# Performance work log

Hardware: AMD Instinct MI355X
Metric: run time of the kernel (lower is better)

Reference implementation:

```python
import jax, jax.numpy as jnp
import numpy as np

MUL0, MUL1 = 128, 64
DIM1 = MUL0 + 3 * MUL1          # 320 = dim of 128x0e + 64x1o
DIM2 = 4                        # 1x0e + 1x1o
WDIM, H = 16, 64
# per-instruction weight sizes (mul_in2 = 1), e3nn instruction order
N1 = MUL0 * MUL0                # (0e x 0e -> 0e)
N2 = MUL0 * MUL1                # (0e x 1o -> 1o)
N3 = MUL1 * MUL1                # (1o x 0e -> 1o)
N4 = MUL1 * MUL0                # (1o x 1o -> 0e)
WNUMEL = N1 + N2 + N3 + N4      # 36864
FAN = MUL0 + MUL1               # summed fan-in per output slice = 192
PW0 = float(np.sqrt(1.0 / FAN))         # path weight, component/element norm, l_out=0
PW1 = float(np.sqrt(3.0 / FAN))         # l_out=1 (alpha = 2l+1 = 3)
INV_SQRT3 = float(1.0 / np.sqrt(3.0))   # wigner_3j(1,1,0)/(0,1,1)/(1,0,1) entries
SQRT_K = float(1.0 / np.sqrt(FAN))      # tp_rescale correction (output divided by this)


def setup_inputs() -> dict:
    key = jax.random.key(0)
    ks = jax.random.split(key, 8)
    N = 4096

    def lin(k, fin, fout):
        k1, k2 = jax.random.split(k)
        lim = 1.0 / np.sqrt(fin)
        W = jax.random.uniform(k1, (fin, fout), minval=-lim, maxval=lim, dtype=jnp.float32)
        b = jax.random.uniform(k2, (fout,), minval=-lim, maxval=lim, dtype=jnp.float32)
        return W, b

    W0, b0 = lin(ks[3], WDIM, H)
    W1, b1 = lin(ks[4], H, H)
    W2, b2 = lin(ks[5], H, WNUMEL)
    return {
        "data_in1": jax.random.normal(ks[0], (N, DIM1), dtype=jnp.float32),
        "data_in2": jax.random.normal(ks[1], (N, DIM2), dtype=jnp.float32),
        "weight": jax.random.normal(ks[2], (N, WDIM), dtype=jnp.float32),
        "W0": W0, "b0": b0, "W1": W1, "b1": b1, "W2": W2, "b2": b2,
        "bias": jax.random.uniform(ks[6], (MUL0,), minval=-SQRT_K, maxval=SQRT_K, dtype=jnp.float32),
    }


def _forward(data_in1, data_in2, weight, W0, b0, W1, b1, W2, b2, bias):
    # weight-generating MLP: 16 -> 64 -> 64 -> weight_numel
    h = jax.nn.relu(weight @ W0 + b0)
    h = jax.nn.relu(h @ W1 + b1)
    w = h @ W2 + b2                                   # [N, WNUMEL] per-sample tp weights
    # split inputs into irrep blocks
    s1 = data_in1[:, :MUL0]                           # [N,128]  128x0e
    v1 = data_in1[:, MUL0:].reshape(-1, MUL1, 3)      # [N,64,3]  64x1o
    s2 = data_in2[:, 0]                               # [N]       1x0e
    v2 = data_in2[:, 1:4]                             # [N,3]     1x1o
    # per-instruction weight views (uvw with v=1 collapsed)
    Wa = w[:, :N1].reshape(-1, MUL0, MUL0)                   # 0e x 0e -> 0e
    Wb = w[:, N1:N1 + N2].reshape(-1, MUL0, MUL1)            # 0e x 1o -> 1o
    Wc = w[:, N1 + N2:N1 + N2 + N3].reshape(-1, MUL1, MUL1)  # 1o x 0e -> 1o
    Wd = w[:, N1 + N2 + N3:].reshape(-1, MUL1, MUL0)         # 1o x 1o -> 0e
    dot12 = jnp.einsum('eui,ei->eu', v1, v2)          # [N,64]
    # scalar (0e) output slice: paths Wa (w3j=1) and Wd (w3j = delta/sqrt(3))
    out0 = PW0 * (jnp.einsum('euw,eu->ew', Wa, s1) * s2[:, None]
                  + INV_SQRT3 * jnp.einsum('euw,eu->ew', Wd, dot12))
    # vector (1o) output slice: paths Wb and Wc (w3j = delta/sqrt(3))
    out1 = PW1 * INV_SQRT3 * (
        jnp.einsum('euw,eu->ew', Wb, s1)[:, :, None] * v2[:, None, :]
        + jnp.einsum('euw,eui->ewi', Wc, v1) * s2[:, None, None])
    out = jnp.concatenate([out0, out1.reshape(-1, 3 * MUL1)], axis=1)  # [N,320]
    out = out / SQRT_K                                # tp_rescale: divide by sqrt_k correction
    out = out.at[:, :MUL0].add(bias)                  # bias added on 0e slice only
    return out


def reference(data_in1, data_in2, weight, W0, b0, W1, b1, W2, b2, bias):
    return _forward(data_in1, data_in2, weight, W0, b0, W1, b1, W2, b2, bias)
```

## Files before the change

### kernel.cpp

```cpp
#include <hip/hip_runtime.h>
#include <hip/hip_bf16.h>

typedef __attribute__((ext_vector_type(8))) short short8;
typedef __attribute__((ext_vector_type(4))) float f32x4;

constexpr int N1 = 16384, N2 = 8192, N3 = 4096;
constexpr int WN = 36864;
constexpr float ISQ3 = 0.57735026918962576451f;

__device__ __forceinline__ unsigned short f2bf(float f) {
  unsigned u = __builtin_bit_cast(unsigned, f);
  u += 0x7fffu + ((u >> 16) & 1u);
  return (unsigned short)(u >> 16);
}

#define MFMA(a, b, c) __builtin_amdgcn_mfma_f32_16x16x32_bf16((a), (b), (c), 0, 0, 0)

__global__ __launch_bounds__(256)
void k_prep(const float* __restrict__ wgt, const float* __restrict__ W0,
            const float* __restrict__ b0, const float* __restrict__ W1,
            const float* __restrict__ b1, const float* __restrict__ W2,
            const float* __restrict__ b2, const float* __restrict__ bias,
            const float* __restrict__ d1, const float* __restrict__ d2,
            float* __restrict__ H, unsigned short* __restrict__ Bp,
            float* __restrict__ sAg, float* __restrict__ sBg,
            float* __restrict__ sDg, float* __restrict__ sCg,
            float* __restrict__ d2T, float* __restrict__ out) {
  __shared__ __align__(16) float shm[10400];
  const int bid = blockIdx.x;
  const int tid = threadIdx.x;

  if (bid < 512) {
    float* s1s = shm;
    float* v1s = shm + 1024;
    float* dts = shm + 2560;
    float* s2s = shm + 3072;
    float* v2s = shm + 3080;
    const int e0 = bid * 8;
    for (int x = tid; x < 8 * 320; x += 256) {
      int e = x / 320, c = x % 320;
      float v = d1[(size_t)(e0 + e) * 320 + c];
      if (c < 128) s1s[e * 128 + c] = v;
      else { int q = c - 128; v1s[(e * 64 + q / 3) * 3 + q % 3] = v; }
    }
    if (tid < 32) {
      int e = tid >> 2, c = tid & 3;
      float v = d2[(size_t)(e0 + e) * 4 + c];
      if (c == 0) s2s[e] = v; else v2s[e * 3 + c - 1] = v;
    }
    __syncthreads();
    for (int x = tid; x < 8 * 64; x += 256) {
      int e = x >> 6, u = x & 63;
      dts[e * 64 + u] = v1s[(e * 64 + u) * 3] * v2s[e * 3] +
                        v1s[(e * 64 + u) * 3 + 1] * v2s[e * 3 + 1] +
                        v1s[(e * 64 + u) * 3 + 2] * v2s[e * 3 + 2];
    }
    __syncthreads();
    for (int c = tid; c < 320; c += 256) {
      if (c < 128) {
        const int w = c;
        float ta[8] = {0,0,0,0,0,0,0,0}, td[8] = {0,0,0,0,0,0,0,0};
        for (int u = 0; u < 128; ++u) {
          float bv = b2[u * 128 + w];
#pragma unroll
          for (int e = 0; e < 8; ++e) ta[e] = fmaf(s1s[e * 128 + u], bv, ta[e]);
        }
        for (int u = 0; u < 64; ++u) {
          float bv = b2[N1 + N2 + N3 + u * 128 + w];
#pragma unroll
          for (int e = 0; e < 8; ++e) td[e] = fmaf(dts[e * 64 + u], bv, td[e]);
        }
        const float bw = bias[w];
#pragma unroll
        for (int e = 0; e < 8; ++e)
          out[(size_t)(e0 + e) * 320 + c] = fmaf(s2s[e], ta[e], ISQ3 * td[e]) + bw;
      } else {
        const int q = c - 128, w = q / 3, i = q % 3;
        float tb[8] = {0,0,0,0,0,0,0,0}, tc[8] = {0,0,0,0,0,0,0,0};
        for (int u = 0; u < 128; ++u) {
          float bv = b2[N1 + u * 64 + w];
#pragma unroll
          for (int e = 0; e < 8; ++e) tb[e] = fmaf(s1s[e * 128 + u], bv, tb[e]);
        }
        for (int u = 0; u < 64; ++u) {
          float bv = b2[N1 + N2 + u * 64 + w];
#pragma unroll
          for (int e = 0; e < 8; ++e) tc[e] = fmaf(v1s[(e * 64 + u) * 3 + i], bv, tc[e]);
        }
#pragma unroll
        for (int e = 0; e < 8; ++e)
          out[(size_t)(e0 + e) * 320 + c] = tb[e] * v2s[e * 3 + i] + tc[e] * s2s[e];
      }
    }
  } else if (bid < 1664) {
    const int g = (bid - 512) * 256 + tid;
    const int lane = g & 63;
    const int nth = g >> 6;
    const int kh = nth & 1, nt = nth >> 1;
    const int n = nt * 16 + (lane & 15);
    const int k0 = kh * 32 + (lane >> 4) * 8;
    short8 v;
#pragma unroll
    for (int q = 0; q < 8; ++q) v[q] = (short)f2bf(W2[(size_t)(k0 + q) * WN + n]);
    *(short8*)(Bp + (size_t)g * 8) = v;
  } else if (bid < 2688) {
    float* h0s = shm;
    const int r = tid >> 6, jj = tid & 63;
    const int e = (bid - 1664) * 4 + r;
    float a = b0[jj];
#pragma unroll
    for (int i = 0; i < 16; ++i) a = fmaf(wgt[e * 16 + i], W0[i * 64 + jj], a);
    h0s[r * 64 + jj] = fmaxf(a, 0.f);
    __syncthreads();
    float a1 = b1[jj];
#pragma unroll
    for (int i = 0; i < 64; ++i) a1 = fmaf(h0s[r * 64 + i], W1[i * 64 + jj], a1);
    H[e * 64 + jj] = fmaxf(a1, 0.f);
  } else {
    float* d1s = shm;
    float* d2s = shm + 10272;
    const int e0 = (bid - 2688) * 32;
    for (int x = tid; x < 32 * 320; x += 256) {
      int e = x / 320, c = x % 320;
      d1s[e * 321 + c] = d1[(size_t)(e0 + e) * 320 + c];
    }
    if (tid < 128) d2s[tid] = d2[(size_t)e0 * 4 + tid];
    __syncthreads();
    const int e = tid & 31;
    const float s2 = d2s[e * 4 + 0];
    const float w1 = d2s[e * 4 + 1], w2 = d2s[e * 4 + 2], w3 = d2s[e * 4 + 3];
    for (int row = (tid >> 5); row < 516; row += 8) {
      float v; float* dst;
      if (row < 128)      { v = d1s[e * 321 + row] * s2;            dst = sAg + (size_t)row * 4096; }
      else if (row < 256) { v = d1s[e * 321 + (row - 128)];         dst = sBg + (size_t)(row - 128) * 4096; }
      else if (row < 320) { int u = row - 256;
        v = ISQ3 * (d1s[e * 321 + 128 + 3 * u] * w1 + d1s[e * 321 + 129 + 3 * u] * w2 +
                    d1s[e * 321 + 130 + 3 * u] * w3);               dst = sDg + (size_t)u * 4096; }
      else if (row < 512) { v = d1s[e * 321 + 128 + (row - 320)] * s2; dst = sCg + (size_t)(row - 320) * 4096; }
      else                { v = d2s[e * 4 + (row - 512)];           dst = d2T + (size_t)(row - 512) * 4096; }
      dst[e0 + e] = v;
    }
  }
}

__global__ __launch_bounds__(256, 3)
void k_main(const float* __restrict__ sAg, const float* __restrict__ sBg,
            const float* __restrict__ sDg, const float* __restrict__ sCg,
            const float* __restrict__ d2T, const float* __restrict__ H,
            const unsigned short* __restrict__ Bp, float* __restrict__ out) {
  __shared__ __align__(16) float lds[8704];
  const int bid = blockIdx.x, tid = threadIdx.x;
  const int wid = tid >> 6, lane = tid & 63;
  const int nl = lane & 15, grp = lane >> 4;
  const short8* Bp8 = (const short8*)Bp;
  const f32x4 Z = {0.f, 0.f, 0.f, 0.f};

  if (bid < 512) {
    const int j = bid & 7, tile = bid >> 3, e0 = tile * 64;
    short8 h00, h01, h10, h11, h20, h21, h30, h31;
    {
      const float* hp; short8 v0, v1;
#define LOADH(EF, N0, N1_)                                                     \
      hp = H + (size_t)(e0 + 16 * EF + nl) * 64 + grp * 8;                     \
      _Pragma("unroll") for (int q = 0; q < 8; ++q) {                          \
        v0[q] = (short)f2bf(hp[q]); v1[q] = (short)f2bf(hp[32 + q]); }         \
      N0 = v0; N1_ = v1;
      LOADH(0, h00, h01) LOADH(1, h10, h11) LOADH(2, h20, h21) LOADH(3, h30, h31)
#undef LOADH
    }
    const int uA0 = wid * 32, uD0 = wid * 16;
    const short8* pA = Bp8 + (size_t)(uA0 * 8 + j) * 128 + lane;
    const short8* pD = Bp8 + (size_t)(1792 + uD0 * 8 + j) * 128 + lane;
    const float* qA0 = sAg + (size_t)uA0 * 4096 + e0 + nl;
    const float* qA1 = qA0 + 4096;
    const float* qD  = sDg + (size_t)uD0 * 4096 + e0 + nl;

    short8 A00 = pA[0], A01 = pA[64], A10 = pA[1024], A11 = pA[1088]; pA += 2048;
    short8 D00 = pD[0], D01 = pD[64]; pD += 1024;
    float sa0 = qA0[0], sa1 = qA0[16], sa2 = qA0[32], sa3 = qA0[48];
    float sa4 = qA1[0], sa5 = qA1[16], sa6 = qA1[32], sa7 = qA1[48]; qA0 += 8192; qA1 += 8192;
    float sd0 = qD[0], sd1 = qD[16], sd2 = qD[32], sd3 = qD[48]; qD += 4096;
    short8 B00 = pA[0], B01 = pA[64], B10 = pA[1024], B11 = pA[1088]; pA += 2048;
    short8 E00 = pD[0], E01 = pD[64]; pD += 1024;
    float ta0 = qA0[0], ta1 = qA0[16], ta2 = qA0[32], ta3 = qA0[48];
    float ta4 = qA1[0], ta5 = qA1[16], ta6 = qA1[32], ta7 = qA1[48]; qA0 += 8192; qA1 += 8192;
    float td0 = qD[0], td1 = qD[16], td2 = qD[32], td3 = qD[48]; qD += 4096;

    f32x4 accA[4] = {Z, Z, Z, Z};
    f32x4 accD[4] = {Z, Z, Z, Z};

#define QUAD(P0, P1, S0, S1, S2, S3, AC) do { f32x4 t_;                        \
    t_ = Z; t_ = MFMA(P0, h00, t_); t_ = MFMA(P1, h01, t_); AC[0] += (S0) * t_; \
    t_ = Z; t_ = MFMA(P0, h10, t_); t_ = MFMA(P1, h11, t_); AC[1] += (S1) * t_; \
    t_ = Z; t_ = MFMA(P0, h20, t_); t_ = MFMA(P1, h21, t_); AC[2] += (S2) * t_; \
    t_ = Z; t_ = MFMA(P0, h30, t_); t_ = MFMA(P1, h31, t_); AC[3] += (S3) * t_; } while (0)

#pragma unroll
    for (int t = 0; t < 16; t += 2) {
      QUAD(A00, A01, sa0, sa1, sa2, sa3, accA);
      QUAD(A10, A11, sa4, sa5, sa6, sa7, accA);
      QUAD(D00, D01, sd0, sd1, sd2, sd3, accD);
      if (t < 14) {
        A00 = pA[0]; A01 = pA[64]; A10 = pA[1024]; A11 = pA[1088]; pA += 2048;
        D00 = pD[0]; D01 = pD[64]; pD += 1024;
        sa0 = qA0[0]; sa1 = qA0[16]; sa2 = qA0[32]; sa3 = qA0[48];
        sa4 = qA1[0]; sa5 = qA1[16]; sa6 = qA1[32]; sa7 = qA1[48]; qA0 += 8192; qA1 += 8192;
        sd0 = qD[0]; sd1 = qD[16]; sd2 = qD[32]; sd3 = qD[48]; qD += 4096;
      }
      QUAD(B00, B01, ta0, ta1, ta2, ta3, accA);
      QUAD(B10, B11, ta4, ta5, ta6, ta7, accA);
      QUAD(E00, E01, td0, td1, td2, td3, accD);
      if (t < 13) {
        B00 = pA[0]; B01 = pA[64]; B10 = pA[1024]; B11 = pA[1088]; pA += 2048;
        E00 = pD[0]; E01 = pD[64]; pD += 1024;
        ta0 = qA0[0]; ta1 = qA0[16]; ta2 = qA0[32]; ta3 = qA0[48];
        ta4 = qA1[0]; ta5 = qA1[16]; ta6 = qA1[32]; ta7 = qA1[48]; qA0 += 8192; qA1 += 8192;
        td0 = qD[0]; td1 = qD[16]; td2 = qD[32]; td3 = qD[48]; qD += 4096;
      }
    }
#undef QUAD

#pragma unroll
    for (int eF = 0; eF < 4; ++eF) {
      f32x4 fin = accA[eF] + accD[eF];
      *(f32x4*)&lds[wid * 1280 + (16 * eF + nl) * 20 + grp * 4] = fin;
    }
    __syncthreads();
    {
      const int e = tid >> 2, w4 = (tid & 3) * 4;
      f32x4 s = Z;
#pragma unroll
      for (int wv = 0; wv < 4; ++wv) s += *(const f32x4*)&lds[wv * 1280 + e * 20 + w4];
      f32x4* op = (f32x4*)(out + (size_t)(e0 + e) * 320 + j * 16 + w4);
      *op = *op + s;
    }
  } else {
    const int idx = bid - 512;
    const int j = idx & 3;
    const int tile = ((idx >> 3) << 1) + ((idx >> 2) & 1);
    const int e0 = tile * 32;
    short8 h00, h01, h10, h11;
    {
      const float* hp; short8 v0, v1;
#define LOADH(EF, N0, N1_)                                                     \
      hp = H + (size_t)(e0 + 16 * EF + nl) * 64 + grp * 8;                     \
      _Pragma("unroll") for (int q = 0; q < 8; ++q) {                          \
        v0[q] = (short)f2bf(hp[q]); v1[q] = (short)f2bf(hp[32 + q]); }         \
      N0 = v0; N1_ = v1;
      LOADH(0, h00, h01) LOADH(1, h10, h11)
#undef LOADH
    }
    const int uB0 = wid * 32, uC0 = wid * 16;
    const short8* pB = Bp8 + (size_t)(1024 + uB0 * 4 + j) * 128 + lane;
    const short8* pC = Bp8 + (size_t)(1536 + uC0 * 4 + j) * 128 + lane;
    const float* qB0 = sBg + (size_t)uB0 * 4096 + e0 + nl;
    const float* qB1 = qB0 + 4096;
    const float* qC0 = sCg + (size_t)(uC0 * 3) * 4096 + e0 + nl;
    const float* qC1 = qC0 + 4096;
    const float* qC2 = qC0 + 8192;

    short8 A00 = pB[0], A01 = pB[64], A10 = pB[512], A11 = pB[576]; pB += 1024;
    short8 C00 = pC[0], C01 = pC[64]; pC += 512;
    float sb0 = qB0[0], sb1 = qB0[16], sb2 = qB1[0], sb3 = qB1[16]; qB0 += 8192; qB1 += 8192;
    float sc00 = qC0[0], sc01 = qC0[16], sc10 = qC1[0], sc11 = qC1[16],
          sc20 = qC2[0], sc21 = qC2[16]; qC0 += 12288; qC1 += 12288; qC2 += 12288;
    short8 B00 = pB[0], B01 = pB[64], B10 = pB[512], B11 = pB[576]; pB += 1024;
    short8 E00 = pC[0], E01 = pC[64]; pC += 512;
    float tb0 = qB0[0], tb1 = qB0[16], tb2 = qB1[0], tb3 = qB1[16]; qB0 += 8192; qB1 += 8192;
    float tc00 = qC0[0], tc01 = qC0[16], tc10 = qC1[0], tc11 = qC1[16],
          tc20 = qC2[0], tc21 = qC2[16]; qC0 += 12288; qC1 += 12288; qC2 += 12288;

    f32x4 accB[2] = {Z, Z};
    f32x4 accC0[2] = {Z, Z}, accC1[2] = {Z, Z}, accC2[2] = {Z, Z};

#define DUO(P0, P1, S0, S1) do { f32x4 t_;                                     \
    t_ = Z; t_ = MFMA(P0, h00, t_); t_ = MFMA(P1, h01, t_); accB[0] += (S0) * t_; \
    t_ = Z; t_ = MFMA(P0, h10, t_); t_ = MFMA(P1, h11, t_); accB[1] += (S1) * t_; } while (0)
#define CTRIO(P0, P1, X00, X01, X10, X11, X20, X21) do { f32x4 u0_, u1_;       \
    u0_ = Z; u0_ = MFMA(P0, h00, u0_); u0_ = MFMA(P1, h01, u0_);               \
    u1_ = Z; u1_ = MFMA(P0, h10, u1_); u1_ = MFMA(P1, h11, u1_);               \
    accC0[0] += (X00) * u0_; accC0[1] += (X01) * u1_;                          \
    accC1[0] += (X10) * u0_; accC1[1] += (X11) * u1_;                          \
    accC2[0] += (X20) * u0_; accC2[1] += (X21) * u1_; } while (0)

#pragma unroll
    for (int t = 0; t < 16; t += 2) {
      DUO(A00, A01, sb0, sb1);
      DUO(A10, A11, sb2, sb3);
      CTRIO(C00, C01, sc00, sc01, sc10, sc11, sc20, sc21);
      if (t < 14) {
        A00 = pB[0]; A01 = pB[64]; A10 = pB[512]; A11 = pB[576]; pB += 1024;
        C00 = pC[0]; C01 = pC[64]; pC += 512;
        sb0 = qB0[0]; sb1 = qB0[16]; sb2 = qB1[0]; sb3 = qB1[16]; qB0 += 8192; qB1 += 8192;
        sc00 = qC0[0]; sc01 = qC0[16]; sc10 = qC1[0]; sc11 = qC1[16];
        sc20 = qC2[0]; sc21 = qC2[16]; qC0 += 12288; qC1 += 12288; qC2 += 12288;
      }
      DUO(B00, B01, tb0, tb1);
      DUO(B10, B11, tb2, tb3);
      CTRIO(E00, E01, tc00, tc01, tc10, tc11, tc20, tc21);
      if (t < 13) {
        B00 = pB[0]; B01 = pB[64]; B10 = pB[512]; B11 = pB[576]; pB += 1024;
        E00 = pC[0]; E01 = pC[64]; pC += 512;
        tb0 = qB0[0]; tb1 = qB0[16]; tb2 = qB1[0]; tb3 = qB1[16]; qB0 += 8192; qB1 += 8192;
        tc00 = qC0[0]; tc01 = qC0[16]; tc10 = qC1[0]; tc11 = qC1[16];
        tc20 = qC2[0]; tc21 = qC2[16]; qC0 += 12288; qC1 += 12288; qC2 += 12288;
      }
    }
#undef DUO
#undef CTRIO

#pragma unroll
    for (int eF = 0; eF < 2; ++eF)
#pragma unroll
      for (int r = 0; r < 4; ++r) {
        f32x4 v = {accB[eF][r], accC0[eF][r], accC1[eF][r], accC2[eF][r]};
        *(f32x4*)&lds[wid * 2176 + (16 * eF + nl) * 68 + (grp * 4 + r) * 4] = v;
      }
    __syncthreads();
    for (int p = tid; p < 512; p += 256) {
      const int e = p >> 4, w = p & 15;
      f32x4 s = Z;
#pragma unroll
      for (int wv = 0; wv < 4; ++wv) s += *(const f32x4*)&lds[wv * 2176 + e * 68 + w * 4];
      const float v20 = d2T[4096 + e0 + e], v21 = d2T[8192 + e0 + e], v22 = d2T[12288 + e0 + e];
      float* op = out + (size_t)(e0 + e) * 320 + 128 + (size_t)(j * 16 + w) * 3;
      op[0] += s[0] * v20 + s[1];
      op[1] += s[0] * v21 + s[2];
      op[2] += s[0] * v22 + s[3];
    }
  }
}

extern "C" void kernel_launch(void* const* d_in, const int* in_sizes, int n_in,
                              void* d_out, int out_size, void* d_ws, size_t ws_size,
                              hipStream_t stream) {
  const float* d1   = (const float*)d_in[0];
  const float* d2   = (const float*)d_in[1];
  const float* wgt  = (const float*)d_in[2];
  const float* W0   = (const float*)d_in[3];
  const float* b0   = (const float*)d_in[4];
  const float* W1   = (const float*)d_in[5];
  const float* b1   = (const float*)d_in[6];
  const float* W2   = (const float*)d_in[7];
  const float* b2   = (const float*)d_in[8];
  const float* bias = (const float*)d_in[9];
  float* out = (float*)d_out;

  char* ws = (char*)d_ws;
  float* H           = (float*)(ws);
  unsigned short* Bp = (unsigned short*)(ws + (1u << 20));
  float* sAg         = (float*)(ws + (6u << 20));
  float* sBg         = (float*)(ws + (8u << 20));
  float* sDg         = (float*)(ws + (10u << 20));
  float* sCg         = (float*)(ws + (11u << 20));
  float* d2T         = (float*)(ws + (14u << 20));

  k_prep<<<2816, 256, 0, stream>>>(wgt, W0, b0, W1, b1, W2, b2, bias, d1, d2,
                                   H, Bp, sAg, sBg, sDg, sCg, d2T, out);
  k_main<<<1024, 256, 0, stream>>>(sAg, sBg, sDg, sCg, d2T, H, Bp, out);
}
```

Baseline: 73.86 us.

## Fold per-sample scalars into MFMA operand and merge all paths into one block

Moves the per-edge scalar multiply into the bf16 H operand: each edge's scaled H row is packed with v_cvt_pk_bf16_f32, so the Wa, Wb and Wd paths accumulate directly in MFMA accumulators instead of scaling each partial product. The Wc path still scales afterwards. One 512-thread block now handles all four paths for a 32-edge tile and half of the output columns, and the two waves sharing each slice are reduced through LDS. It also adds s_setprio around the MFMA bursts and cuts the grid to 256 blocks, which trades per-step VALU packing and lower occupancy for fewer scalar multiply-adds and fewer launched blocks.

```diff
diff --git a/kernel.cpp b/kernel.cpp
--- a/kernel.cpp
+++ b/kernel.cpp
@@ -3,6 +3,7 @@
 
 typedef __attribute__((ext_vector_type(8))) short short8;
 typedef __attribute__((ext_vector_type(4))) float f32x4;
+typedef __attribute__((ext_vector_type(4))) unsigned uint4v;
 
 constexpr int N1 = 16384, N2 = 8192, N3 = 4096;
 constexpr int WN = 36864;
@@ -14,7 +15,22 @@
   return (unsigned short)(u >> 16);
 }
 
+__device__ __forceinline__ unsigned pkbf(float a, float b) {
+  unsigned r;
+  asm("v_cvt_pk_bf16_f32 %0, %1, %2" : "=v"(r) : "v"(a), "v"(b));
+  return r;
+}
+
 #define MFMA(a, b, c) __builtin_amdgcn_mfma_f32_16x16x32_bf16((a), (b), (c), 0, 0, 0)
+
+#define SYNTH(S, HF, G0, G1) do {                                                   \
+    uint4v w0_, w1_;                                                                \
+    w0_[0] = pkbf((S)*HF[0],  (S)*HF[1]);   w0_[1] = pkbf((S)*HF[2],  (S)*HF[3]);   \
+    w0_[2] = pkbf((S)*HF[4],  (S)*HF[5]);   w0_[3] = pkbf((S)*HF[6],  (S)*HF[7]);   \
+    w1_[0] = pkbf((S)*HF[8],  (S)*HF[9]);   w1_[1] = pkbf((S)*HF[10], (S)*HF[11]);  \
+    w1_[2] = pkbf((S)*HF[12], (S)*HF[13]);  w1_[3] = pkbf((S)*HF[14], (S)*HF[15]);  \
+    G0 = __builtin_bit_cast(short8, w0_);   G1 = __builtin_bit_cast(short8, w1_);   \
+  } while (0)
 
 __global__ __launch_bounds__(256)
 void k_prep(const float* __restrict__ wgt, const float* __restrict__ W0,
@@ -143,190 +159,255 @@
   }
 }
 
-__global__ __launch_bounds__(256, 3)
+
+#define ADBODY(F0,F1,F2,F3,F4,F5,F6,F7,S0,S1) do {                             \
+    short8 g00,g01,g10,g11;                                                    \
+    SYNTH(S0, hf0, g00, g01); SYNTH(S1, hf1, g10, g11);                        \
+    __builtin_amdgcn_s_setprio(1);                                             \
+    a00 = MFMA(F0,g00,a00); a00 = MFMA(F1,g01,a00);                            \
+    a01 = MFMA(F0,g10,a01); a01 = MFMA(F1,g11,a01);                            \
+    a10 = MFMA(F2,g00,a10); a10 = MFMA(F3,g01,a10);                            \
+    a11 = MFMA(F2,g10,a11); a11 = MFMA(F3,g11,a11);                            \
+    a20 = MFMA(F4,g00,a20); a20 = MFMA(F5,g01,a20);                            \
+    a21 = MFMA(F4,g10,a21); a21 = MFMA(F5,g11,a21);                            \
+    a30 = MFMA(F6,g00,a30); a30 = MFMA(F7,g01,a30);                            \
+    a31 = MFMA(F6,g10,a31); a31 = MFMA(F7,g11,a31);                            \
+    __builtin_amdgcn_s_setprio(0);                                             \
+  } while (0)
+
+#define BBODY(F0,F1,F2,F3,S0,S1) do {                                          \
+    short8 g00,g01,g10,g11;                                                    \
+    SYNTH(S0, hf0, g00, g01); SYNTH(S1, hf1, g10, g11);                        \
+    __builtin_amdgcn_s_setprio(1);                                             \
+    b00 = MFMA(F0,g00,b00); b00 = MFMA(F1,g01,b00);                            \
+    b01 = MFMA(F0,g10,b01); b01 = MFMA(F1,g11,b01);                            \
+    b10 = MFMA(F2,g00,b10); b10 = MFMA(F3,g01,b10);                            \
+    b11 = MFMA(F2,g10,b11); b11 = MFMA(F3,g11,b11);                            \
+    __builtin_amdgcn_s_setprio(0);                                             \
+  } while (0)
+
+#define CBODY(F0,F1,F2,F3,S00,S01,S10,S11,S20,S21) do {                        \
+    __builtin_amdgcn_s_setprio(1);                                             \
+    f32x4 t00 = Zv; t00 = MFMA(F0,hb00,t00); t00 = MFMA(F1,hb01,t00);          \
+    f32x4 t01 = Zv; t01 = MFMA(F0,hb10,t01); t01 = MFMA(F1,hb11,t01);          \
+    f32x4 t10 = Zv; t10 = MFMA(F2,hb00,t10); t10 = MFMA(F3,hb01,t10);          \
+    f32x4 t11 = Zv; t11 = MFMA(F2,hb10,t11); t11 = MFMA(F3,hb11,t11);          \
+    __builtin_amdgcn_s_setprio(0);                                             \
+    c000 += S00*t00; c001 += S01*t01; c010 += S00*t10; c011 += S01*t11;        \
+    c100 += S10*t00; c101 += S11*t01; c110 += S10*t10; c111 += S11*t11;        \
+    c200 += S20*t00; c201 += S21*t01; c210 += S20*t10; c211 += S21*t11;        \
+  } while (0)
+
+__global__ __launch_bounds__(512, 2)
 void k_main(const float* __restrict__ sAg, const float* __restrict__ sBg,
             const float* __restrict__ sDg, const float* __restrict__ sCg,
             const float* __restrict__ d2T, const float* __restrict__ H,
             const unsigned short* __restrict__ Bp, float* __restrict__ out) {
-  __shared__ __align__(16) float lds[8704];
-  const int bid = blockIdx.x, tid = threadIdx.x;
+  __shared__ __align__(16) float buf[4 * 32 * 136];
+  const int tid = threadIdx.x;
   const int wid = tid >> 6, lane = tid & 63;
   const int nl = lane & 15, grp = lane >> 4;
+  const int h = (blockIdx.x >> 2) & 1;
+  const int tile = (blockIdx.x >> 3) * 4 + (blockIdx.x & 3);
+  const int e0 = tile * 32;
   const short8* Bp8 = (const short8*)Bp;
-  const f32x4 Z = {0.f, 0.f, 0.f, 0.f};
-
-  if (bid < 512) {
-    const int j = bid & 7, tile = bid >> 3, e0 = tile * 64;
-    short8 h00, h01, h10, h11, h20, h21, h30, h31;
-    {
-      const float* hp; short8 v0, v1;
-#define LOADH(EF, N0, N1_)                                                     \
-      hp = H + (size_t)(e0 + 16 * EF + nl) * 64 + grp * 8;                     \
-      _Pragma("unroll") for (int q = 0; q < 8; ++q) {                          \
-        v0[q] = (short)f2bf(hp[q]); v1[q] = (short)f2bf(hp[32 + q]); }         \
-      N0 = v0; N1_ = v1;
-      LOADH(0, h00, h01) LOADH(1, h10, h11) LOADH(2, h20, h21) LOADH(3, h30, h31)
-#undef LOADH
-    }
-    const int uA0 = wid * 32, uD0 = wid * 16;
-    const short8* pA = Bp8 + (size_t)(uA0 * 8 + j) * 128 + lane;
-    const short8* pD = Bp8 + (size_t)(1792 + uD0 * 8 + j) * 128 + lane;
-    const float* qA0 = sAg + (size_t)uA0 * 4096 + e0 + nl;
-    const float* qA1 = qA0 + 4096;
-    const float* qD  = sDg + (size_t)uD0 * 4096 + e0 + nl;
-
-    short8 A00 = pA[0], A01 = pA[64], A10 = pA[1024], A11 = pA[1088]; pA += 2048;
-    short8 D00 = pD[0], D01 = pD[64]; pD += 1024;
-    float sa0 = qA0[0], sa1 = qA0[16], sa2 = qA0[32], sa3 = qA0[48];
-    float sa4 = qA1[0], sa5 = qA1[16], sa6 = qA1[32], sa7 = qA1[48]; qA0 += 8192; qA1 += 8192;
-    float sd0 = qD[0], sd1 = qD[16], sd2 = qD[32], sd3 = qD[48]; qD += 4096;
-    short8 B00 = pA[0], B01 = pA[64], B10 = pA[1024], B11 = pA[1088]; pA += 2048;
-    short8 E00 = pD[0], E01 = pD[64]; pD += 1024;
-    float ta0 = qA0[0], ta1 = qA0[16], ta2 = qA0[32], ta3 = qA0[48];
-    float ta4 = qA1[0], ta5 = qA1[16], ta6 = qA1[32], ta7 = qA1[48]; qA0 += 8192; qA1 += 8192;
-    float td0 = qD[0], td1 = qD[16], td2 = qD[32], td3 = qD[48]; qD += 4096;
-
-    f32x4 accA[4] = {Z, Z, Z, Z};
-    f32x4 accD[4] = {Z, Z, Z, Z};
-
-#define QUAD(P0, P1, S0, S1, S2, S3, AC) do { f32x4 t_;                        \
-    t_ = Z; t_ = MFMA(P0, h00, t_); t_ = MFMA(P1, h01, t_); AC[0] += (S0) * t_; \
-    t_ = Z; t_ = MFMA(P0, h10, t_); t_ = MFMA(P1, h11, t_); AC[1] += (S1) * t_; \
-    t_ = Z; t_ = MFMA(P0, h20, t_); t_ = MFMA(P1, h21, t_); AC[2] += (S2) * t_; \
-    t_ = Z; t_ = MFMA(P0, h30, t_); t_ = MFMA(P1, h31, t_); AC[3] += (S3) * t_; } while (0)
-
-#pragma unroll
-    for (int t = 0; t < 16; t += 2) {
-      QUAD(A00, A01, sa0, sa1, sa2, sa3, accA);
-      QUAD(A10, A11, sa4, sa5, sa6, sa7, accA);
-      QUAD(D00, D01, sd0, sd1, sd2, sd3, accD);
-      if (t < 14) {
-        A00 = pA[0]; A01 = pA[64]; A10 = pA[1024]; A11 = pA[1088]; pA += 2048;
-        D00 = pD[0]; D01 = pD[64]; pD += 1024;
-        sa0 = qA0[0]; sa1 = qA0[16]; sa2 = qA0[32]; sa3 = qA0[48];
-        sa4 = qA1[0]; sa5 = qA1[16]; sa6 = qA1[32]; sa7 = qA1[48]; qA0 += 8192; qA1 += 8192;
-        sd0 = qD[0]; sd1 = qD[16]; sd2 = qD[32]; sd3 = qD[48]; qD += 4096;
-      }
-      QUAD(B00, B01, ta0, ta1, ta2, ta3, accA);
-      QUAD(B10, B11, ta4, ta5, ta6, ta7, accA);
-      QUAD(E00, E01, td0, td1, td2, td3, accD);
-      if (t < 13) {
-        B00 = pA[0]; B01 = pA[64]; B10 = pA[1024]; B11 = pA[1088]; pA += 2048;
-        E00 = pD[0]; E01 = pD[64]; pD += 1024;
-        ta0 = qA0[0]; ta1 = qA0[16]; ta2 = qA0[32]; ta3 = qA0[48];
-        ta4 = qA1[0]; ta5 = qA1[16]; ta6 = qA1[32]; ta7 = qA1[48]; qA0 += 8192; qA1 += 8192;
-        td0 = qD[0]; td1 = qD[16]; td2 = qD[32]; td3 = qD[48]; qD += 4096;
-      }
-    }
-#undef QUAD
-
-#pragma unroll
-    for (int eF = 0; eF < 4; ++eF) {
-      f32x4 fin = accA[eF] + accD[eF];
-      *(f32x4*)&lds[wid * 1280 + (16 * eF + nl) * 20 + grp * 4] = fin;
-    }
-    __syncthreads();
-    {
-      const int e = tid >> 2, w4 = (tid & 3) * 4;
-      f32x4 s = Z;
-#pragma unroll
-      for (int wv = 0; wv < 4; ++wv) s += *(const f32x4*)&lds[wv * 1280 + e * 20 + w4];
-      f32x4* op = (f32x4*)(out + (size_t)(e0 + e) * 320 + j * 16 + w4);
-      *op = *op + s;
-    }
-  } else {
-    const int idx = bid - 512;
-    const int j = idx & 3;
-    const int tile = ((idx >> 3) << 1) + ((idx >> 2) & 1);
-    const int e0 = tile * 32;
-    short8 h00, h01, h10, h11;
-    {
-      const float* hp; short8 v0, v1;
-#define LOADH(EF, N0, N1_)                                                     \
-      hp = H + (size_t)(e0 + 16 * EF + nl) * 64 + grp * 8;                     \
-      _Pragma("unroll") for (int q = 0; q < 8; ++q) {                          \
-        v0[q] = (short)f2bf(hp[q]); v1[q] = (short)f2bf(hp[32 + q]); }         \
-      N0 = v0; N1_ = v1;
-      LOADH(0, h00, h01) LOADH(1, h10, h11)
-#undef LOADH
-    }
-    const int uB0 = wid * 32, uC0 = wid * 16;
-    const short8* pB = Bp8 + (size_t)(1024 + uB0 * 4 + j) * 128 + lane;
-    const short8* pC = Bp8 + (size_t)(1536 + uC0 * 4 + j) * 128 + lane;
-    const float* qB0 = sBg + (size_t)uB0 * 4096 + e0 + nl;
-    const float* qB1 = qB0 + 4096;
-    const float* qC0 = sCg + (size_t)(uC0 * 3) * 4096 + e0 + nl;
-    const float* qC1 = qC0 + 4096;
-    const float* qC2 = qC0 + 8192;
-
-    short8 A00 = pB[0], A01 = pB[64], A10 = pB[512], A11 = pB[576]; pB += 1024;
-    short8 C00 = pC[0], C01 = pC[64]; pC += 512;
-    float sb0 = qB0[0], sb1 = qB0[16], sb2 = qB1[0], sb3 = qB1[16]; qB0 += 8192; qB1 += 8192;
-    float sc00 = qC0[0], sc01 = qC0[16], sc10 = qC1[0], sc11 = qC1[16],
-          sc20 = qC2[0], sc21 = qC2[16]; qC0 += 12288; qC1 += 12288; qC2 += 12288;
-    short8 B00 = pB[0], B01 = pB[64], B10 = pB[512], B11 = pB[576]; pB += 1024;
-    short8 E00 = pC[0], E01 = pC[64]; pC += 512;
-    float tb0 = qB0[0], tb1 = qB0[16], tb2 = qB1[0], tb3 = qB1[16]; qB0 += 8192; qB1 += 8192;
-    float tc00 = qC0[0], tc01 = qC0[16], tc10 = qC1[0], tc11 = qC1[16],
-          tc20 = qC2[0], tc21 = qC2[16]; qC0 += 12288; qC1 += 12288; qC2 += 12288;
-
-    f32x4 accB[2] = {Z, Z};
-    f32x4 accC0[2] = {Z, Z}, accC1[2] = {Z, Z}, accC2[2] = {Z, Z};
-
-#define DUO(P0, P1, S0, S1) do { f32x4 t_;                                     \
-    t_ = Z; t_ = MFMA(P0, h00, t_); t_ = MFMA(P1, h01, t_); accB[0] += (S0) * t_; \
-    t_ = Z; t_ = MFMA(P0, h10, t_); t_ = MFMA(P1, h11, t_); accB[1] += (S1) * t_; } while (0)
-#define CTRIO(P0, P1, X00, X01, X10, X11, X20, X21) do { f32x4 u0_, u1_;       \
-    u0_ = Z; u0_ = MFMA(P0, h00, u0_); u0_ = MFMA(P1, h01, u0_);               \
-    u1_ = Z; u1_ = MFMA(P0, h10, u1_); u1_ = MFMA(P1, h11, u1_);               \
-    accC0[0] += (X00) * u0_; accC0[1] += (X01) * u1_;                          \
-    accC1[0] += (X10) * u0_; accC1[1] += (X11) * u1_;                          \
-    accC2[0] += (X20) * u0_; accC2[1] += (X21) * u1_; } while (0)
-
-#pragma unroll
-    for (int t = 0; t < 16; t += 2) {
-      DUO(A00, A01, sb0, sb1);
-      DUO(A10, A11, sb2, sb3);
-      CTRIO(C00, C01, sc00, sc01, sc10, sc11, sc20, sc21);
-      if (t < 14) {
-        A00 = pB[0]; A01 = pB[64]; A10 = pB[512]; A11 = pB[576]; pB += 1024;
-        C00 = pC[0]; C01 = pC[64]; pC += 512;
-        sb0 = qB0[0]; sb1 = qB0[16]; sb2 = qB1[0]; sb3 = qB1[16]; qB0 += 8192; qB1 += 8192;
-        sc00 = qC0[0]; sc01 = qC0[16]; sc10 = qC1[0]; sc11 = qC1[16];
-        sc20 = qC2[0]; sc21 = qC2[16]; qC0 += 12288; qC1 += 12288; qC2 += 12288;
-      }
-      DUO(B00, B01, tb0, tb1);
-      DUO(B10, B11, tb2, tb3);
-      CTRIO(E00, E01, tc00, tc01, tc10, tc11, tc20, tc21);
-      if (t < 13) {
-        B00 = pB[0]; B01 = pB[64]; B10 = pB[512]; B11 = pB[576]; pB += 1024;
-        E00 = pC[0]; E01 = pC[64]; pC += 512;
-        tb0 = qB0[0]; tb1 = qB0[16]; tb2 = qB1[0]; tb3 = qB1[16]; qB0 += 8192; qB1 += 8192;
-        tc00 = qC0[0]; tc01 = qC0[16]; tc10 = qC1[0]; tc11 = qC1[16];
-        tc20 = qC2[0]; tc21 = qC2[16]; qC0 += 12288; qC1 += 12288; qC2 += 12288;
-      }
-    }
-#undef DUO
-#undef CTRIO
-
-#pragma unroll
-    for (int eF = 0; eF < 2; ++eF)
-#pragma unroll
-      for (int r = 0; r < 4; ++r) {
-        f32x4 v = {accB[eF][r], accC0[eF][r], accC1[eF][r], accC2[eF][r]};
-        *(f32x4*)&lds[wid * 2176 + (16 * eF + nl) * 68 + (grp * 4 + r) * 4] = v;
-      }
-    __syncthreads();
-    for (int p = tid; p < 512; p += 256) {
-      const int e = p >> 4, w = p & 15;
-      f32x4 s = Z;
-#pragma unroll
-      for (int wv = 0; wv < 4; ++wv) s += *(const f32x4*)&lds[wv * 2176 + e * 68 + w * 4];
+  const f32x4 Zv = {0.f, 0.f, 0.f, 0.f};
+
+  float hf0[16], hf1[16];
+  {
+    const float* hp0 = H + (size_t)(e0 + nl) * 64 + grp * 8;
+    const float* hp1 = H + (size_t)(e0 + 16 + nl) * 64 + grp * 8;
+    f32x4 x0 = *(const f32x4*)(hp0),      x1 = *(const f32x4*)(hp0 + 4);
+    f32x4 x2 = *(const f32x4*)(hp0 + 32), x3 = *(const f32x4*)(hp0 + 36);
+    f32x4 y0 = *(const f32x4*)(hp1),      y1 = *(const f32x4*)(hp1 + 4);
+    f32x4 y2 = *(const f32x4*)(hp1 + 32), y3 = *(const f32x4*)(hp1 + 36);
+#pragma unroll
+    for (int q = 0; q < 4; ++q) {
+      hf0[q] = x0[q]; hf0[4+q] = x1[q]; hf0[8+q] = x2[q]; hf0[12+q] = x3[q];
+      hf1[q] = y0[q]; hf1[4+q] = y1[q]; hf1[8+q] = y2[q]; hf1[12+q] = y3[q];
+    }
+  }
+
+  f32x4 a00=Zv,a01=Zv,a10=Zv,a11=Zv,a20=Zv,a21=Zv,a30=Zv,a31=Zv;
+
+  {
+    const int u0 = wid * 16;
+    const short8* pe = Bp8 + (size_t)(u0 * 8 + 4 * h) * 128 + lane;
+    const short8* po = pe + 1024;
+    const float* se = sAg + (size_t)u0 * 4096 + e0 + nl;
+    const float* so = se + 4096;
+    short8 Ea0=pe[0],Ea1=pe[64],Ea2=pe[128],Ea3=pe[192],Ea4=pe[256],Ea5=pe[320],Ea6=pe[384],Ea7=pe[448];
+    short8 Oa0=po[0],Oa1=po[64],Oa2=po[128],Oa3=po[192],Oa4=po[256],Oa5=po[320],Oa6=po[384],Oa7=po[448];
+    float sE0=se[0], sE1=se[16], sO0=so[0], sO1=so[16];
+#pragma unroll 2
+    for (int t = 0; t < 8; ++t) {
+      ADBODY(Ea0,Ea1,Ea2,Ea3,Ea4,Ea5,Ea6,Ea7, sE0,sE1);
+      pe += 2048; se += 8192;
+      Ea0=pe[0];Ea1=pe[64];Ea2=pe[128];Ea3=pe[192];Ea4=pe[256];Ea5=pe[320];Ea6=pe[384];Ea7=pe[448];
+      sE0=se[0]; sE1=se[16];
+      ADBODY(Oa0,Oa1,Oa2,Oa3,Oa4,Oa5,Oa6,Oa7, sO0,sO1);
+      po += 2048; so += 8192;
+      Oa0=po[0];Oa1=po[64];Oa2=po[128];Oa3=po[192];Oa4=po[256];Oa5=po[320];Oa6=po[384];Oa7=po[448];
+      sO0=so[0]; sO1=so[16];
+    }
+  }
+
+  f32x4 b00=Zv,b01=Zv,b10=Zv,b11=Zv;
+
+  {
+    const int u0 = wid * 16;
+    const short8* pe = Bp8 + (size_t)(1024 + u0 * 4 + 2 * h) * 128 + lane;
+    const short8* po = pe + 512;
+    const float* se = sBg + (size_t)u0 * 4096 + e0 + nl;
+    const float* so = se + 4096;
+    short8 Ea0=pe[0],Ea1=pe[64],Ea2=pe[128],Ea3=pe[192];
+    short8 Oa0=po[0],Oa1=po[64],Oa2=po[128],Oa3=po[192];
+    float sE0=se[0], sE1=se[16], sO0=so[0], sO1=so[16];
+#pragma unroll 2
+    for (int t = 0; t < 8; ++t) {
+      BBODY(Ea0,Ea1,Ea2,Ea3, sE0,sE1);
+      pe += 1024; se += 8192;
+      Ea0=pe[0];Ea1=pe[64];Ea2=pe[128];Ea3=pe[192];
+      sE0=se[0]; sE1=se[16];
+      BBODY(Oa0,Oa1,Oa2,Oa3, sO0,sO1);
+      po += 1024; so += 8192;
+      Oa0=po[0];Oa1=po[64];Oa2=po[128];Oa3=po[192];
+      sO0=so[0]; sO1=so[16];
+    }
+  }
+
+  {
+    const int u0 = wid * 8;
+    const short8* pe = Bp8 + (size_t)(1792 + u0 * 8 + 4 * h) * 128 + lane;
+    const short8* po = pe + 1024;
+    const float* se = sDg + (size_t)u0 * 4096 + e0 + nl;
+    const float* so = se + 4096;
+    short8 Ea0=pe[0],Ea1=pe[64],Ea2=pe[128],Ea3=pe[192],Ea4=pe[256],Ea5=pe[320],Ea6=pe[384],Ea7=pe[448];
+    short8 Oa0=po[0],Oa1=po[64],Oa2=po[128],Oa3=po[192],Oa4=po[256],Oa5=po[320],Oa6=po[384],Oa7=po[448];
+    float sE0=se[0], sE1=se[16], sO0=so[0], sO1=so[16];
+#pragma unroll 2
+    for (int t = 0; t < 4; ++t) {
+      ADBODY(Ea0,Ea1,Ea2,Ea3,Ea4,Ea5,Ea6,Ea7, sE0,sE1);
+      pe += 2048; se += 8192;
+      Ea0=pe[0];Ea1=pe[64];Ea2=pe[128];Ea3=pe[192];Ea4=pe[256];Ea5=pe[320];Ea6=pe[384];Ea7=pe[448];
+      sE0=se[0]; sE1=se[16];
+      ADBODY(Oa0,Oa1,Oa2,Oa3,Oa4,Oa5,Oa6,Oa7, sO0,sO1);
+      po += 2048; so += 8192;
+      Oa0=po[0];Oa1=po[64];Oa2=po[128];Oa3=po[192];Oa4=po[256];Oa5=po[320];Oa6=po[384];Oa7=po[448];
+      sO0=so[0]; sO1=so[16];
+    }
+  }
+
+  short8 hb00, hb01, hb10, hb11;
+  SYNTH(1.0f, hf0, hb00, hb01);
+  SYNTH(1.0f, hf1, hb10, hb11);
+  f32x4 c000=Zv,c001=Zv,c010=Zv,c011=Zv,c100=Zv,c101=Zv,c110=Zv,c111=Zv,c200=Zv,c201=Zv,c210=Zv,c211=Zv;
+  {
+    const int u0 = wid * 8;
+    const short8* pe = Bp8 + (size_t)(1536 + u0 * 4 + 2 * h) * 128 + lane;
+    const short8* po = pe + 512;
+    const float* sc0e = sCg + (size_t)(3 * u0) * 4096 + e0 + nl;
+    const float* sc1e = sc0e + 4096;
+    const float* sc2e = sc0e + 8192;
+    const float* sc0o = sc0e + 12288;
+    const float* sc1o = sc0e + 16384;
+    const float* sc2o = sc0e + 20480;
+    short8 Ea0=pe[0],Ea1=pe[64],Ea2=pe[128],Ea3=pe[192];
+    short8 Oa0=po[0],Oa1=po[64],Oa2=po[128],Oa3=po[192];
+    float sE00=sc0e[0],sE01=sc0e[16],sE10=sc1e[0],sE11=sc1e[16],sE20=sc2e[0],sE21=sc2e[16];
+    float sO00=sc0o[0],sO01=sc0o[16],sO10=sc1o[0],sO11=sc1o[16],sO20=sc2o[0],sO21=sc2o[16];
+#pragma unroll 2
+    for (int t = 0; t < 4; ++t) {
+      CBODY(Ea0,Ea1,Ea2,Ea3, sE00,sE01,sE10,sE11,sE20,sE21);
+      pe += 1024; sc0e += 24576; sc1e += 24576; sc2e += 24576;
+      Ea0=pe[0];Ea1=pe[64];Ea2=pe[128];Ea3=pe[192];
+      sE00=sc0e[0];sE01=sc0e[16];sE10=sc1e[0];sE11=sc1e[16];sE20=sc2e[0];sE21=sc2e[16];
+      CBODY(Oa0,Oa1,Oa2,Oa3, sO00,sO01,sO10,sO11,sO20,sO21);
+      po += 1024; sc0o += 24576; sc1o += 24576; sc2o += 24576;
+      Oa0=po[0];Oa1=po[64];Oa2=po[128];Oa3=po[192];
+      sO00=sc0o[0];sO01=sc0o[16];sO10=sc1o[0];sO11=sc1o[16];sO20=sc2o[0];sO21=sc2o[16];
+    }
+  }
+
+  {
+    f32x4 av[8] = {a00,a01,a10,a11,a20,a21,a30,a31};
+    const int ew = (wid & 3) * 2080;
+    if (wid >= 4) {
+#pragma unroll
+      for (int j = 0; j < 4; ++j)
+#pragma unroll
+        for (int eF = 0; eF < 2; ++eF) {
+          float* p = &buf[ew + (eF * 16 + nl) * 65 + j * 16 + grp * 4];
+#pragma unroll
+          for (int r = 0; r < 4; ++r) p[r] = av[j * 2 + eF][r];
+        }
+    }
+    __syncthreads();
+    if (wid < 4) {
+#pragma unroll
+      for (int j = 0; j < 4; ++j)
+#pragma unroll
+        for (int eF = 0; eF < 2; ++eF) {
+          float* p = &buf[ew + (eF * 16 + nl) * 65 + j * 16 + grp * 4];
+#pragma unroll
+          for (int r = 0; r < 4; ++r) p[r] += av[j * 2 + eF][r];
+        }
+    }
+    __syncthreads();
+#pragma unroll
+    for (int it = 0; it < 4; ++it) {
+      const int p = tid + it * 512;
+      const int e = p >> 6, s = p & 63;
+      float v = buf[e * 65 + s] + buf[2080 + e * 65 + s] +
+                buf[4160 + e * 65 + s] + buf[6240 + e * 65 + s];
+      out[(size_t)(e0 + e) * 320 + 64 * h + s] += v;
+    }
+    __syncthreads();
+  }
+  {
+    f32x4 bv[4] = {b00,b01,b10,b11};
+    f32x4 cv[12] = {c000,c001,c010,c011,c100,c101,c110,c111,c200,c201,c210,c211};
+    const int ew = (wid & 3) * 4352;
+    if (wid >= 4) {
+#pragma unroll
+      for (int j = 0; j < 2; ++j)
+#pragma unroll
+        for (int eF = 0; eF < 2; ++eF)
+#pragma unroll
+          for (int r = 0; r < 4; ++r) {
+            const int w1 = j * 16 + grp * 4 + r;
+            f32x4 st = {bv[j*2+eF][r], cv[j*2+eF][r], cv[4 + j*2+eF][r], cv[8 + j*2+eF][r]};
+            *(f32x4*)&buf[ew + (eF * 16 + nl) * 136 + w1 * 4] = st;
+          }
+    }
+    __syncthreads();
+    if (wid < 4) {
+#pragma unroll
+      for (int j = 0; j < 2; ++j)
+#pragma unroll
+        for (int eF = 0; eF < 2; ++eF)
+#pragma unroll
+          for (int r = 0; r < 4; ++r) {
+            const int w1 = j * 16 + grp * 4 + r;
+            f32x4* p = (f32x4*)&buf[ew + (eF * 16 + nl) * 136 + w1 * 4];
+            f32x4 st = {bv[j*2+eF][r], cv[j*2+eF][r], cv[4 + j*2+eF][r], cv[8 + j*2+eF][r]};
+            *p = *p + st;
+          }
+    }
+    __syncthreads();
+#pragma unroll
+    for (int it = 0; it < 2; ++it) {
+      const int p = tid + it * 512;
+      const int e = p >> 5, w1 = p & 31;
+      f32x4 v = *(const f32x4*)&buf[e * 136 + w1 * 4];
+      v += *(const f32x4*)&buf[4352 + e * 136 + w1 * 4];
+      v += *(const f32x4*)&buf[8704 + e * 136 + w1 * 4];
+      v += *(const f32x4*)&buf[13056 + e * 136 + w1 * 4];
       const float v20 = d2T[4096 + e0 + e], v21 = d2T[8192 + e0 + e], v22 = d2T[12288 + e0 + e];
-      float* op = out + (size_t)(e0 + e) * 320 + 128 + (size_t)(j * 16 + w) * 3;
-      op[0] += s[0] * v20 + s[1];
-      op[1] += s[0] * v21 + s[2];
-      op[2] += s[0] * v22 + s[3];
+      float* op = out + (size_t)(e0 + e) * 320 + 128 + (size_t)(32 * h + w1) * 3;
+      op[0] += v[0] * v20 + v[1];
+      op[1] += v[0] * v21 + v[2];
+      op[2] += v[0] * v22 + v[3];
     }
   }
 }
@@ -357,5 +438,5 @@
 
   k_prep<<<2816, 256, 0, stream>>>(wgt, W0, b0, W1, b1, W2, b2, bias, d1, d2,
                                    H, Bp, sAg, sBg, sDg, sCg, d2T, out);
-  k_main<<<1024, 256, 0, stream>>>(sAg, sBg, sDg, sCg, d2T, H, Bp, out);
+  k_main<<<256, 512, 0, stream>>>(sAg, sBg, sDg, sCg, d2T, H, Bp, out);
 }
```

After: 67.71 us. 1.09x faster.
